# Kernel tuning notes

Hardware: AMD Instinct MI355X
Metric: run time of the kernel (lower is better)

## Reference

```python
import jax, jax.numpy as jnp
import numpy as np

H = 1024      # hidden_size
V = 32000     # vocab_size
MAX_LEN = 32  # decode steps
B = 64        # batch


def _uni(key, shape, s):
    return jax.random.uniform(key, shape, jnp.float32, -s, s)


def setup_inputs() -> dict:
    key = jax.random.key(0)
    ks = jax.random.split(key, 10)
    s = 1.0 / np.sqrt(H)
    return {
        "vectors": jax.random.normal(ks[0], (B, H), jnp.float32),
        "W_fc_in": _uni(ks[1], (H, H), s),
        "b_fc_in": _uni(ks[2], (H,), s),
        "W_ih": _uni(ks[3], (3 * H, H), s),   # torch GRU weight_ih_l0 (r,z,n)
        "W_hh": _uni(ks[4], (3 * H, H), s),
        "b_ih": _uni(ks[5], (3 * H,), s),
        "b_hh": _uni(ks[6], (3 * H,), s),
        "W_out": _uni(ks[7], (V, H), s),
        "b_out": _uni(ks[8], (V,), s),
        "top_k": 8,
    }


def reference(vectors, W_fc_in, b_fc_in, W_ih, W_hh, b_ih, b_hh, W_out, b_out, top_k):
    # hidden = fc_in(vectors); initial GRU input is zeros
    h0 = vectors @ W_fc_in.T + b_fc_in           # [B, H]
    x0 = jnp.zeros_like(h0)

    def gru_cell(carry, _):
        h, x = carry
        gi = x @ W_ih.T + b_ih                   # [B, 3H]
        gh = h @ W_hh.T + b_hh                   # [B, 3H]
        i_r, i_z, i_n = jnp.split(gi, 3, axis=-1)
        h_r, h_z, h_n = jnp.split(gh, 3, axis=-1)
        r = jax.nn.sigmoid(i_r + h_r)
        z = jax.nn.sigmoid(i_z + h_z)
        n = jnp.tanh(i_n + r * h_n)
        h_new = (1.0 - z) * n + z * h            # PyTorch GRU update
        # out == h_new for single-layer GRU; inputs = out feeds back
        return (h_new, h_new), h_new

    _, outs = jax.lax.scan(gru_cell, (h0, x0), None, length=MAX_LEN)  # [T, B, H]

    # fc_out + log_softmax over vocab, for all steps at once
    logits = jnp.einsum('tbh,vh->tbv', outs, W_out) + b_out           # [T, B, V]
    logp = jax.nn.log_softmax(logits, axis=-1)

    # topk then multinomial over exp(top logp) == categorical over top logp
    top_p, top_i = jax.lax.top_k(logp, top_k)                         # [T, B, K]
    samp = jax.random.categorical(jax.random.key(42), top_p, axis=-1)  # [T, B]
    tokens = jnp.take_along_axis(top_i, samp[..., None], axis=-1)[..., 0]
    return tokens.T.astype(jnp.int32)                                  # [B, T]
```

## Files before the change

### kernel.cpp

```cpp
#include <hip/hip_runtime.h>
#include <stdint.h>

typedef unsigned int u32;
typedef unsigned long long u64;
typedef unsigned short ushort;
typedef __attribute__((ext_vector_type(8))) short bf16x8;
typedef __attribute__((ext_vector_type(4))) float f32x4;

#define JAX_PARTITIONABLE 1

#define HD     1024
#define BBATCH 64
#define TSTEP  32
#define VOCAB  32000
#define NROWS  2048
#define GATE6  6144
#define NCB    250
#define NCAND  16

__device__ __forceinline__ void threefry2x32(u32 k0, u32 k1, u32 x0, u32 x1,
                                             u32& y0, u32& y1) {
  u32 ks2 = k0 ^ k1 ^ 0x1BD11BDAu;
  x0 += k0; x1 += k1;
#define TFR(r) do { x0 += x1; x1 = (x1 << (r)) | (x1 >> (32 - (r))); x1 ^= x0; } while (0)
  TFR(13); TFR(15); TFR(26); TFR(6);   x0 += k1;  x1 += ks2 + 1u;
  TFR(17); TFR(29); TFR(16); TFR(24);  x0 += ks2; x1 += k0 + 2u;
  TFR(13); TFR(15); TFR(26); TFR(6);   x0 += k0;  x1 += k1 + 3u;
  TFR(17); TFR(29); TFR(16); TFR(24);  x0 += k1;  x1 += ks2 + 4u;
  TFR(13); TFR(15); TFR(26); TFR(6);   x0 += ks2; x1 += k0 + 5u;
#undef TFR
  y0 = x0; y1 = x1;
}

__device__ __forceinline__ u32 jax_random_bits(u32 n) {
#if JAX_PARTITIONABLE
  u32 y0, y1; threefry2x32(0u, 42u, 0u, n, y0, y1);
  return y0 ^ y1;
#else
  u32 y0, y1;
  if (n < 8192u) { threefry2x32(0u, 42u, n, n + 8192u, y0, y1); return y0; }
  else           { threefry2x32(0u, 42u, n - 8192u, n, y0, y1); return y1; }
#endif
}

__device__ __forceinline__ u64 packkey(float v, int idx) {
  u32 b = __float_as_uint(v);
  b = (b & 0x80000000u) ? ~b : (b | 0x80000000u);
  return ((u64)b << 32) | (u64)(~(u32)idx);
}

__device__ __forceinline__ void insert4(u64* t4, u64 k) {
  if (k > t4[3]) {
    t4[3] = k;
    if (t4[3] > t4[2]) { u64 tm = t4[2]; t4[2] = t4[3]; t4[3] = tm; }
    if (t4[2] > t4[1]) { u64 tm = t4[1]; t4[1] = t4[2]; t4[2] = tm; }
    if (t4[1] > t4[0]) { u64 tm = t4[0]; t4[0] = t4[1]; t4[1] = tm; }
  }
}

__device__ __forceinline__ ushort f2bf_rne(float x) {
  u32 u = __float_as_uint(x);
  return (ushort)((u + 0x7fffu + ((u >> 16) & 1u)) >> 16);
}
__device__ __forceinline__ float bf2f(ushort h) {
  return __uint_as_float(((u32)h) << 16);
}

typedef const __attribute__((address_space(1))) void* gas_ptr;
typedef __attribute__((address_space(3))) void* las_ptr;
__device__ __forceinline__ void gload16(const void* g, void* l) {
  __builtin_amdgcn_global_load_lds((gas_ptr)g, (las_ptr)l, 16, 0, 0);
}

__global__ __launch_bounds__(256) void tobf16(const float* __restrict__ src,
                                              ushort* __restrict__ dst, int n8) {
  int i = blockIdx.x * 256 + threadIdx.x;
  const int stride = gridDim.x * 256;
  for (; i < n8; i += stride) {
    const float4* s4 = (const float4*)src + (size_t)i * 2;
    float4 a = s4[0], b = s4[1];
    u32 o0 = f2bf_rne(a.x) | ((u32)f2bf_rne(a.y) << 16);
    u32 o1 = f2bf_rne(a.z) | ((u32)f2bf_rne(a.w) << 16);
    u32 o2 = f2bf_rne(b.x) | ((u32)f2bf_rne(b.y) << 16);
    u32 o3 = f2bf_rne(b.z) | ((u32)f2bf_rne(b.w) << 16);
    ((uint4*)dst)[i] = make_uint4(o0, o1, o2, o3);
  }
}

__global__ __launch_bounds__(256) void tobf16x3_gru(
    const float* __restrict__ Wih, const float* __restrict__ Whh,
    ushort* __restrict__ w1, ushort* __restrict__ w2, ushort* __restrict__ w3,
    int n8) {
  int i = blockIdx.x * 256 + threadIdx.x;
  const int stride = gridDim.x * 256;
  const int half = 3072 * HD / 8;
  for (; i < n8; i += stride) {
    const float4* s4 = (i < half) ? ((const float4*)Wih + (size_t)i * 2)
                                  : ((const float4*)Whh + (size_t)(i - half) * 2);
    float v[8];
    float4 a = s4[0], b = s4[1];
    v[0]=a.x; v[1]=a.y; v[2]=a.z; v[3]=a.w; v[4]=b.x; v[5]=b.y; v[6]=b.z; v[7]=b.w;
    ushort p1[8], p2[8], p3[8];
#pragma unroll
    for (int e = 0; e < 8; ++e) {
      p1[e] = f2bf_rne(v[e]);
      float r1 = v[e] - bf2f(p1[e]);
      p2[e] = f2bf_rne(r1);
      float r2 = r1 - bf2f(p2[e]);
      p3[e] = f2bf_rne(r2);
    }
    u32 o1[4], o2[4], o3[4];
#pragma unroll
    for (int e = 0; e < 4; ++e) {
      o1[e] = p1[2*e] | ((u32)p1[2*e+1] << 16);
      o2[e] = p2[2*e] | ((u32)p2[2*e+1] << 16);
      o3[e] = p3[2*e] | ((u32)p3[2*e+1] << 16);
    }
    ((uint4*)w1)[i] = make_uint4(o1[0], o1[1], o1[2], o1[3]);
    ((uint4*)w2)[i] = make_uint4(o2[0], o2[1], o2[2], o2[3]);
    ((uint4*)w3)[i] = make_uint4(o3[0], o3[1], o3[2], o3[3]);
  }
}

__global__ __launch_bounds__(256) void gemm64_nt(
    const float* __restrict__ A, const float* __restrict__ B,
    float* __restrict__ part) {
  __shared__ float4 As4[64 * 33];
  __shared__ float4 Bs4[32 * 33];
  const int tid = threadIdx.x;
  const int n0 = blockIdx.x * 32;
  const float* Brow = B + (size_t)n0 * HD;
  const int ks = blockIdx.y * 256;
  const int tc = tid & 7, trg = tid >> 3;
  float acc[2][4] = {};
  for (int kc = 0; kc < 2; ++kc) {
    const int k0 = ks + kc * 128;
#pragma unroll
    for (int l = 0; l < 8; ++l) {
      int m = tid + l * 256; int row = m >> 5, k4 = m & 31;
      As4[row * 33 + k4] = *(const float4*)(A + (size_t)row * HD + k0 + k4 * 4);
    }
#pragma unroll
    for (int l = 0; l < 4; ++l) {
      int m = tid + l * 256; int row = m >> 5, k4 = m & 31;
      Bs4[row * 33 + k4] = *(const float4*)(Brow + (size_t)row * HD + k0 + k4 * 4);
    }
    __syncthreads();
#pragma unroll
    for (int kq = 0; kq < 32; ++kq) {
      float4 av[2], bv[4];
      av[0] = As4[trg * 33 + kq];
      av[1] = As4[(trg + 32) * 33 + kq];
      bv[0] = Bs4[tc * 33 + kq];
      bv[1] = Bs4[(tc + 8) * 33 + kq];
      bv[2] = Bs4[(tc + 16) * 33 + kq];
      bv[3] = Bs4[(tc + 24) * 33 + kq];
#pragma unroll
      for (int i = 0; i < 2; ++i)
#pragma unroll
        for (int j = 0; j < 4; ++j) {
          acc[i][j] += av[i].x * bv[j].x;
          acc[i][j] += av[i].y * bv[j].y;
          acc[i][j] += av[i].z * bv[j].z;
          acc[i][j] += av[i].w * bv[j].w;
        }
    }
    __syncthreads();
  }
  float* P = part + (size_t)blockIdx.y * BBATCH * HD;
#pragma unroll
  for (int i = 0; i < 2; ++i) {
    int b = trg + 32 * i;
#pragma unroll
    for (int j = 0; j < 4; ++j)
      P[(size_t)b * HD + n0 + tc + 8 * j] = acc[i][j];
  }
}

__global__ __launch_bounds__(256) void combine_fcin(
    const float* __restrict__ part, const float* __restrict__ b_fc,
    float* __restrict__ h, ushort* __restrict__ h1, ushort* __restrict__ h2,
    ushort* __restrict__ h3) {
  int idx = blockIdx.x * 256 + threadIdx.x;
  int j = idx & 1023; int b = idx >> 10;
  const size_t S = (size_t)BBATCH * HD;
  const float* p = part + (size_t)b * HD;
  float d = p[j]; d += p[S + j]; d += p[2 * S + j]; d += p[3 * S + j];
  float hv = d + b_fc[j];
  h[idx] = hv;
  ushort a = f2bf_rne(hv);
  float r1 = hv - bf2f(a);
  ushort bb = f2bf_rne(r1);
  float r2 = r1 - bf2f(bb);
  h1[idx] = a; h2[idx] = bb; h3[idx] = f2bf_rne(r2);
}

__global__ __launch_bounds__(256) void gru_gemm(
    const ushort* __restrict__ h1, const ushort* __restrict__ h2,
    const ushort* __restrict__ h3,
    const ushort* __restrict__ W1, const ushort* __restrict__ W2,
    const ushort* __restrict__ W3,
    int colBase, float* __restrict__ g2) {
  __shared__ ushort A1s[64 * 64], A2s[64 * 64], A3s[64 * 64];
  __shared__ ushort B1s[32 * 64], B2s[32 * 64], B3s[32 * 64];
  const int tid = threadIdx.x;
  const int lane = tid & 63, wid = tid >> 6;
  const int wr = wid >> 1, wc = wid & 1;
  const int n0 = colBase + blockIdx.x * 32;
  const int kb0 = blockIdx.y * 512;
  const ushort* B1g = W1 + (size_t)n0 * HD;
  const ushort* B2g = W2 + (size_t)n0 * HD;
  const ushort* B3g = W3 + (size_t)n0 * HD;
  const int rc = lane >> 3;
  const int gr8 = ((lane & 7) ^ rc) * 8;
  const int l15 = lane & 15;
  const int kseg = (lane >> 4) * 16;

  f32x4 acc[2];
  acc[0] = (f32x4){0.f, 0.f, 0.f, 0.f};
  acc[1] = (f32x4){0.f, 0.f, 0.f, 0.f};

  for (int kt = 0; kt < 8; ++kt) {
    const int k0 = kb0 + kt * 64;
#pragma unroll
    for (int c = 0; c < 9; ++c) {
      int q = wid * 9 + c;
      const ushort* src; ushort* dst; int cl;
      if (q < 8)       { cl = q;      src = h1 + (size_t)(cl*8+rc) * HD;  dst = A1s + cl*512; }
      else if (q < 16) { cl = q - 8;  src = h2 + (size_t)(cl*8+rc) * HD;  dst = A2s + cl*512; }
      else if (q < 24) { cl = q - 16; src = h3 + (size_t)(cl*8+rc) * HD;  dst = A3s + cl*512; }
      else if (q < 28) { cl = q - 24; src = B1g + (size_t)(cl*8+rc) * HD; dst = B1s + cl*512; }
      else if (q < 32) { cl = q - 28; src = B2g + (size_t)(cl*8+rc) * HD; dst = B2s + cl*512; }
      else             { cl = q - 32; src = B3g + (size_t)(cl*8+rc) * HD; dst = B3s + cl*512; }
      gload16(src + k0 + gr8, dst);
    }
    asm volatile("s_waitcnt vmcnt(0)" ::: "memory");
    __syncthreads();
#pragma unroll
    for (int ks = 0; ks < 2; ++ks) {
      const int kb = ks * 64 + kseg;
      bf16x8 a1[2], a2[2], a3[2], b1, b2, b3;
#pragma unroll
      for (int m = 0; m < 2; ++m) {
        int row = wr * 32 + m * 16 + l15;
        int off = row * 128 + (kb ^ ((row & 7) << 4));
        a1[m] = *(const bf16x8*)((const char*)A1s + off);
        a2[m] = *(const bf16x8*)((const char*)A2s + off);
        a3[m] = *(const bf16x8*)((const char*)A3s + off);
      }
      {
        int row = wc * 16 + l15;
        int off = row * 128 + (kb ^ ((row & 7) << 4));
        b1 = *(const bf16x8*)((const char*)B1s + off);
        b2 = *(const bf16x8*)((const char*)B2s + off);
        b3 = *(const bf16x8*)((const char*)B3s + off);
      }
#pragma unroll
      for (int m = 0; m < 2; ++m) {
        acc[m] = __builtin_amdgcn_mfma_f32_16x16x32_bf16(a3[m], b1, acc[m], 0, 0, 0);
        acc[m] = __builtin_amdgcn_mfma_f32_16x16x32_bf16(a1[m], b3, acc[m], 0, 0, 0);
        acc[m] = __builtin_amdgcn_mfma_f32_16x16x32_bf16(a2[m], b2, acc[m], 0, 0, 0);
        acc[m] = __builtin_amdgcn_mfma_f32_16x16x32_bf16(a2[m], b1, acc[m], 0, 0, 0);
        acc[m] = __builtin_amdgcn_mfma_f32_16x16x32_bf16(a1[m], b2, acc[m], 0, 0, 0);
        acc[m] = __builtin_amdgcn_mfma_f32_16x16x32_bf16(a1[m], b1, acc[m], 0, 0, 0);
      }
    }
    __syncthreads();
  }
  float* G = g2 + (size_t)blockIdx.y * BBATCH * GATE6;
#pragma unroll
  for (int m = 0; m < 2; ++m)
#pragma unroll
    for (int j = 0; j < 4; ++j) {
      int row = wr * 32 + m * 16 + (lane >> 4) * 4 + j;
      int col = n0 + wc * 16 + l15;
      G[(size_t)row * GATE6 + col] = acc[m][j];
    }
}

__global__ __launch_bounds__(256) void gru_gate2(
    const float* __restrict__ g2, const float* __restrict__ b_ih,
    const float* __restrict__ b_hh, float* __restrict__ h,
    float* __restrict__ outs, ushort* __restrict__ outs_bf,
    ushort* __restrict__ h1, ushort* __restrict__ h2, ushort* __restrict__ h3,
    int t, int first) {
  int idx = blockIdx.x * 256 + threadIdx.x;
  int b = idx >> 10, j = idx & 1023;
  const size_t S = (size_t)BBATCH * GATE6;
  const float* p = g2 + (size_t)b * GATE6;
  float gir, giz, gin;
  if (first) {
    gir = b_ih[j]; giz = b_ih[HD + j]; gin = b_ih[2 * HD + j];
  } else {
    gir = p[j]        + p[S + j]        + b_ih[j];
    giz = p[HD + j]   + p[S + HD + j]   + b_ih[HD + j];
    gin = p[2*HD + j] + p[S + 2*HD + j] + b_ih[2 * HD + j];
  }
  float ghr = p[3072 + j]        + p[S + 3072 + j]        + b_hh[j];
  float ghz = p[3072 + HD + j]   + p[S + 3072 + HD + j]   + b_hh[HD + j];
  float ghn = p[3072 + 2*HD + j] + p[S + 3072 + 2*HD + j] + b_hh[2 * HD + j];
  float r = 1.0f / (1.0f + expf(-(gir + ghr)));
  float z = 1.0f / (1.0f + expf(-(giz + ghz)));
  float n = tanhf(gin + r * ghn);
  float hp = h[idx];
  float hn = (1.0f - z) * n + z * hp;
  h[idx] = hn;
  size_t o = ((size_t)t * BBATCH + b) * HD + j;
  outs[o] = hn;
  ushort a = f2bf_rne(hn);
  outs_bf[o] = a;
  float r1 = hn - bf2f(a);
  ushort bb = f2bf_rne(r1);
  float r2 = r1 - bf2f(bb);
  h1[idx] = a; h2[idx] = bb; h3[idx] = f2bf_rne(r2);
}

__global__ __launch_bounds__(256) void gemm_out_mfma(
    const ushort* __restrict__ Abf, const ushort* __restrict__ Bbf,
    const float* __restrict__ b_out, u64* __restrict__ keys) {
  __shared__ ushort Asm[128 * 64];
  __shared__ ushort Bsm[128 * 64];
  __shared__ float Cs[32 * 133];
  __shared__ u64 pk[64 * 4];

  const int tid = threadIdx.x;
  const int lane = tid & 63;
  const int wid = tid >> 6;
  const int wr = wid >> 1, wc = wid & 1;
  const int cb = blockIdx.y;
  const int half = blockIdx.x;
  const int n0 = cb * 128;

  const ushort* Bg = Bbf + (size_t)n0 * HD;
  const int rc = lane >> 3;
  const int gr8 = ((lane & 7) ^ rc) * 8;
  const int l15 = lane & 15;
  const int kseg = (lane >> 4) * 16;

  float bo[4];
#pragma unroll
  for (int n = 0; n < 4; ++n) bo[n] = b_out[n0 + wc * 64 + n * 16 + l15];

  for (int rb = 0; rb < 8; ++rb) {
    const int r0 = (half * 8 + rb) * 128;
    const ushort* Ag = Abf + (size_t)r0 * HD;

    f32x4 acc[4][4];
#pragma unroll
    for (int m = 0; m < 4; ++m)
#pragma unroll
      for (int n = 0; n < 4; ++n) acc[m][n] = (f32x4){0.f, 0.f, 0.f, 0.f};

    for (int kt = 0; kt < 16; ++kt) {
      const int k0 = kt * 64;
#pragma unroll
      for (int c = 0; c < 4; ++c) {
        int ch = wid * 4 + c;
        int row = ch * 8 + rc;
        gload16(Ag + (size_t)row * HD + k0 + gr8, Asm + ch * 512);
        gload16(Bg + (size_t)row * HD + k0 + gr8, Bsm + ch * 512);
      }
      asm volatile("s_waitcnt vmcnt(0)" ::: "memory");
      __syncthreads();
#pragma unroll
      for (int ks = 0; ks < 2; ++ks) {
        bf16x8 a[4], b[4];
#pragma unroll
        for (int m = 0; m < 4; ++m) {
          int row = wr * 64 + m * 16 + l15;
          int kb = ks * 64 + kseg;
          int off = row * 128 + (kb ^ ((row & 7) << 4));
          a[m] = *(const bf16x8*)((const char*)Asm + off);
        }
#pragma unroll
        for (int n = 0; n < 4; ++n) {
          int row = wc * 64 + n * 16 + l15;
          int kb = ks * 64 + kseg;
          int off = row * 128 + (kb ^ ((row & 7) << 4));
          b[n] = *(const bf16x8*)((const char*)Bsm + off);
        }
#pragma unroll
        for (int m = 0; m < 4; ++m)
#pragma unroll
          for (int n = 0; n < 4; ++n)
            acc[m][n] = __builtin_amdgcn_mfma_f32_16x16x32_bf16(a[m], b[n], acc[m][n], 0, 0, 0);
      }
      __syncthreads();
    }

    for (int q = 0; q < 4; ++q) {
      if (wr == (q >> 1)) {
        int mbase = (q & 1) * 2;
#pragma unroll
        for (int mi = 0; mi < 2; ++mi) {
          int m = mbase + mi;
#pragma unroll
          for (int n = 0; n < 4; ++n) {
            int c = wc * 64 + n * 16 + l15;
#pragma unroll
            for (int j = 0; j < 4; ++j) {
              int lr = mi * 16 + (lane >> 4) * 4 + j;
              Cs[lr * 133 + c] = acc[m][n][j] + bo[n];
            }
          }
        }
      }
      __syncthreads();
      if (tid < 64) {
        int rr = tid >> 1, hc = (tid & 1) * 64;
        const float* rp = Cs + rr * 133 + hc;
        u64 t4[4] = {0, 0, 0, 0};
        for (int c = 0; c < 64; ++c) insert4(t4, packkey(rp[c], n0 + hc + c));
        u64* d = pk + tid * 4;
        d[0] = t4[0]; d[1] = t4[1]; d[2] = t4[2]; d[3] = t4[3];
      }
      __syncthreads();
      if (tid < 32) {
        const u64* a4 = pk + tid * 8;
        u64 t4[4] = {a4[0], a4[1], a4[2], a4[3]};
        insert4(t4, a4[4]); insert4(t4, a4[5]); insert4(t4, a4[6]); insert4(t4, a4[7]);
        int grow = r0 + q * 32 + tid;
        u64* kp = keys + ((size_t)grow * NCB + cb) * 4;
        kp[0] = t4[0]; kp[1] = t4[1]; kp[2] = t4[2]; kp[3] = t4[3];
      }
      __syncthreads();
    }
  }
}

__global__ __launch_bounds__(256) void merge_sample2(
    const u64* __restrict__ keys, const float* __restrict__ outs,
    const float* __restrict__ W_out, const float* __restrict__ b_out,
    int* __restrict__ out) {
  const int r = blockIdx.x, tid = threadIdx.x;
  const int lane = tid & 63, wid = tid >> 6;
  __shared__ u64 K[1000];
  __shared__ u64 wmax[4];
  __shared__ u64 topw[NCAND];
  __shared__ float candv[NCAND];
  __shared__ float row_f[1024];
  for (int i = tid; i < 1000; i += 256) K[i] = keys[(size_t)r * 1000 + i];
  for (int i = tid; i < 1024; i += 256) row_f[i] = outs[(size_t)r * 1024 + i];
  __syncthreads();
  for (int it = 0; it < NCAND; ++it) {
    u64 b = 0;
#pragma unroll
    for (int l = 0; l < 4; ++l) {
      int i = tid + l * 256;
      if (i < 1000) { u64 v = K[i]; b = (v > b) ? v : b; }
    }
#pragma unroll
    for (int o = 32; o; o >>= 1) {
      u64 x = __shfl_xor(b, o);
      if (x > b) b = x;
    }
    if (lane == 0) wmax[wid] = b;
    __syncthreads();
    u64 w = wmax[0];
    if (wmax[1] > w) w = wmax[1];
    if (wmax[2] > w) w = wmax[2];
    if (wmax[3] > w) w = wmax[3];
    if (tid == 0) topw[it] = w;
#pragma unroll
    for (int l = 0; l < 4; ++l) {
      int i = tid + l * 256;
      if (i < 1000 && K[i] == w) K[i] = 0;
    }
    __syncthreads();
  }
  {
    int c = tid >> 4, l16 = tid & 15;
    int vidx = (int)(~(u32)(topw[c] & 0xffffffffu));
    const float* wrow = W_out + (size_t)vidx * HD;
    float s = 0.f;
    for (int e = l16; e < 1024; e += 16) s += row_f[e] * wrow[e];
#pragma unroll
    for (int o = 8; o; o >>= 1) s += __shfl_xor(s, o, 16);
    if (l16 == 0) candv[c] = s + b_out[vidx];
  }
  __syncthreads();
  if (tid == 0) {
    float v[NCAND]; int vi[NCAND];
#pragma unroll
    for (int q = 0; q < NCAND; ++q) {
      v[q] = candv[q];
      vi[q] = (int)(~(u32)(topw[q] & 0xffffffffu));
    }
    for (int a = 0; a < 8; ++a)
      for (int b2 = a + 1; b2 < NCAND; ++b2) {
        bool sw = (v[b2] > v[a]) || (v[b2] == v[a] && vi[b2] < vi[a]);
        if (sw) {
          float tf = v[a]; v[a] = v[b2]; v[b2] = tf;
          int ti = vi[a]; vi[a] = vi[b2]; vi[b2] = ti;
        }
      }
    const float M = v[0];
    const float TINY = 1.17549435e-38f;
    float best = -3.4e38f; int bi = 0;
    for (int k = 0; k < 8; ++k) {
      float lp = v[k] - M;
      u32 bits = jax_random_bits((u32)(r * 8 + k));
      float f = __uint_as_float((bits >> 9) | 0x3f800000u) - 1.0f;
      float u = f * (1.0f - TINY) + TINY;
      u = fmaxf(TINY, u);
      float g = -logf(-logf(u));
      float s = g + lp;
      if (s > best) { best = s; bi = k; }
    }
    int t = r >> 6, b = r & 63;
    out[b * TSTEP + t] = vi[bi];
  }
}

extern "C" void kernel_launch(void* const* d_in, const int* in_sizes, int n_in,
                              void* d_out, int out_size, void* d_ws, size_t ws_size,
                              hipStream_t stream) {
  (void)in_sizes; (void)n_in; (void)out_size; (void)ws_size;
  const float* vectors = (const float*)d_in[0];
  const float* W_fc_in = (const float*)d_in[1];
  const float* b_fc_in = (const float*)d_in[2];
  const float* W_ih    = (const float*)d_in[3];
  const float* W_hh    = (const float*)d_in[4];
  const float* b_ih    = (const float*)d_in[5];
  const float* b_hh    = (const float*)d_in[6];
  const float* W_out   = (const float*)d_in[7];
  const float* b_out   = (const float*)d_in[8];
  int* out = (int*)d_out;

  char* w = (char*)d_ws;
  float* h = (float*)w;          w += (size_t)BBATCH * HD * 4;
  float* outs = (float*)w;       w += (size_t)NROWS * HD * 4;
  ushort* outs_bf = (ushort*)w;  w += (size_t)NROWS * HD * 2;
  ushort* Wbf = (ushort*)w;      w += (size_t)VOCAB * HD * 2;
  char* X = w;                   w += (size_t)3 * GATE6 * HD * 2;
  ushort* Wg1 = (ushort*)X;
  ushort* Wg2 = Wg1 + (size_t)GATE6 * HD;
  ushort* Wg3 = Wg2 + (size_t)GATE6 * HD;
  u64* keys = (u64*)X;
  ushort* h1 = (ushort*)w;       w += (size_t)BBATCH * HD * 2;
  ushort* h2 = (ushort*)w;       w += (size_t)BBATCH * HD * 2;
  ushort* h3 = (ushort*)w;       w += (size_t)BBATCH * HD * 2;
  float* part = (float*)w;
  float* g2   = (float*)w;

  tobf16<<<4096, 256, 0, stream>>>(W_out, Wbf, VOCAB * HD / 8);
  tobf16x3_gru<<<1024, 256, 0, stream>>>(W_ih, W_hh, Wg1, Wg2, Wg3, GATE6 * HD / 8);

  gemm64_nt<<<dim3(32, 4), 256, 0, stream>>>(vectors, W_fc_in, part);
  combine_fcin<<<256, 256, 0, stream>>>(part, b_fc_in, h, h1, h2, h3);

  for (int t = 0; t < TSTEP; ++t) {
    if (t == 0)
      gru_gemm<<<dim3(96, 2), 256, 0, stream>>>(h1, h2, h3, Wg1, Wg2, Wg3, 3072, g2);
    else
      gru_gemm<<<dim3(192, 2), 256, 0, stream>>>(h1, h2, h3, Wg1, Wg2, Wg3, 0, g2);
    gru_gate2<<<256, 256, 0, stream>>>(g2, b_ih, b_hh, h, outs, outs_bf,
                                       h1, h2, h3, t, t == 0 ? 1 : 0);
  }

  gemm_out_mfma<<<dim3(2, NCB), 256, 0, stream>>>(outs_bf, Wbf, b_out, keys);

  merge_sample2<<<NROWS, 256, 0, stream>>>(keys, outs, W_out, b_out, out);
}
```

Measured before the change: 1.257 ms.

## Fuse GRU steps into persistent kernel with grid barriers; double-buffer output GEMM

Replaces the 64 per-step GEMM and gate launches with one persistent kernel of 384 blocks. Each block computes its gate GEMM tile, waits at a hierarchical atomic grid barrier, applies the gate update, then waits at a second barrier. This removes kernel launch overhead and gaps between steps, but relies on all 384 blocks being resident at once, since the barrier could deadlock otherwise. Separately, the vocab-projection GEMM now uses 32-wide k-tiles double-buffered in LDS with a new swizzle, so global loads overlap MFMA compute.

Result: slower. 4.815 ms (+283.2%).

```diff
diff --git a/kernel.cpp b/kernel.cpp
--- a/kernel.cpp
+++ b/kernel.cpp
@@ -17,6 +17,7 @@
 #define GATE6  6144
 #define NCB    250
 #define NCAND  16
+#define GRU_BLOCKS 384
 
 __device__ __forceinline__ void threefry2x32(u32 k0, u32 k1, u32 x0, u32 x1,
                                              u32& y0, u32& y1) {
@@ -70,6 +71,36 @@
 typedef __attribute__((address_space(3))) void* las_ptr;
 __device__ __forceinline__ void gload16(const void* g, void* l) {
   __builtin_amdgcn_global_load_lds((gas_ptr)g, (las_ptr)l, 16, 0, 0);
+}
+
+__device__ __forceinline__ void grid_bar2(u32* B, int nPerGrp) {
+  __syncthreads();
+  if (threadIdx.x == 0) {
+    __threadfence();
+    const int g = blockIdx.x & 7;
+    u32* gc = B + g * 32;
+    u32* gg = B + 256 + g * 32;
+    u32 mygen = __hip_atomic_load(gg, __ATOMIC_RELAXED, __HIP_MEMORY_SCOPE_AGENT);
+    u32 a = __hip_atomic_fetch_add(gc, 1u, __ATOMIC_ACQ_REL, __HIP_MEMORY_SCOPE_AGENT);
+    if (a == (u32)nPerGrp - 1) {
+      __hip_atomic_store(gc, 0u, __ATOMIC_RELAXED, __HIP_MEMORY_SCOPE_AGENT);
+      u32* GC = B + 512; u32* GG = B + 544;
+      u32 mg = __hip_atomic_load(GG, __ATOMIC_RELAXED, __HIP_MEMORY_SCOPE_AGENT);
+      u32 ga = __hip_atomic_fetch_add(GC, 1u, __ATOMIC_ACQ_REL, __HIP_MEMORY_SCOPE_AGENT);
+      if (ga == 7u) {
+        __hip_atomic_store(GC, 0u, __ATOMIC_RELAXED, __HIP_MEMORY_SCOPE_AGENT);
+        __hip_atomic_fetch_add(GG, 1u, __ATOMIC_RELEASE, __HIP_MEMORY_SCOPE_AGENT);
+      } else {
+        while (__hip_atomic_load(GG, __ATOMIC_ACQUIRE, __HIP_MEMORY_SCOPE_AGENT) == mg)
+          __builtin_amdgcn_s_sleep(1);
+      }
+      __hip_atomic_fetch_add(gg, 1u, __ATOMIC_RELEASE, __HIP_MEMORY_SCOPE_AGENT);
+    } else {
+      while (__hip_atomic_load(gg, __ATOMIC_ACQUIRE, __HIP_MEMORY_SCOPE_AGENT) == mygen)
+        __builtin_amdgcn_s_sleep(1);
+    }
+  }
+  __syncthreads();
 }
 
 __global__ __launch_bounds__(256) void tobf16(const float* __restrict__ src,
@@ -195,19 +226,23 @@
   h1[idx] = a; h2[idx] = bb; h3[idx] = f2bf_rne(r2);
 }
 
-__global__ __launch_bounds__(256) void gru_gemm(
-    const ushort* __restrict__ h1, const ushort* __restrict__ h2,
-    const ushort* __restrict__ h3,
+__global__ __launch_bounds__(256, 2) void gru_fused(
     const ushort* __restrict__ W1, const ushort* __restrict__ W2,
     const ushort* __restrict__ W3,
-    int colBase, float* __restrict__ g2) {
+    const float* __restrict__ b_ih, const float* __restrict__ b_hh,
+    float* __restrict__ h, float* __restrict__ outs,
+    ushort* __restrict__ outs_bf,
+    ushort* __restrict__ h1, ushort* __restrict__ h2, ushort* __restrict__ h3,
+    float* __restrict__ g2, u32* __restrict__ bar) {
   __shared__ ushort A1s[64 * 64], A2s[64 * 64], A3s[64 * 64];
   __shared__ ushort B1s[32 * 64], B2s[32 * 64], B3s[32 * 64];
   const int tid = threadIdx.x;
   const int lane = tid & 63, wid = tid >> 6;
   const int wr = wid >> 1, wc = wid & 1;
-  const int n0 = colBase + blockIdx.x * 32;
-  const int kb0 = blockIdx.y * 512;
+  const int bid = blockIdx.x;
+  const int n0 = (bid >> 1) * 32;
+  const int ksplit = bid & 1;
+  const int kb0 = ksplit * 512;
   const ushort* B1g = W1 + (size_t)n0 * HD;
   const ushort* B2g = W2 + (size_t)n0 * HD;
   const ushort* B3g = W3 + (size_t)n0 * HD;
@@ -215,111 +250,111 @@
   const int gr8 = ((lane & 7) ^ rc) * 8;
   const int l15 = lane & 15;
   const int kseg = (lane >> 4) * 16;
-
-  f32x4 acc[2];
-  acc[0] = (f32x4){0.f, 0.f, 0.f, 0.f};
-  acc[1] = (f32x4){0.f, 0.f, 0.f, 0.f};
-
-  for (int kt = 0; kt < 8; ++kt) {
-    const int k0 = kb0 + kt * 64;
-#pragma unroll
-    for (int c = 0; c < 9; ++c) {
-      int q = wid * 9 + c;
-      const ushort* src; ushort* dst; int cl;
-      if (q < 8)       { cl = q;      src = h1 + (size_t)(cl*8+rc) * HD;  dst = A1s + cl*512; }
-      else if (q < 16) { cl = q - 8;  src = h2 + (size_t)(cl*8+rc) * HD;  dst = A2s + cl*512; }
-      else if (q < 24) { cl = q - 16; src = h3 + (size_t)(cl*8+rc) * HD;  dst = A3s + cl*512; }
-      else if (q < 28) { cl = q - 24; src = B1g + (size_t)(cl*8+rc) * HD; dst = B1s + cl*512; }
-      else if (q < 32) { cl = q - 28; src = B2g + (size_t)(cl*8+rc) * HD; dst = B2s + cl*512; }
-      else             { cl = q - 32; src = B3g + (size_t)(cl*8+rc) * HD; dst = B3s + cl*512; }
-      gload16(src + k0 + gr8, dst);
-    }
-    asm volatile("s_waitcnt vmcnt(0)" ::: "memory");
-    __syncthreads();
-#pragma unroll
-    for (int ks = 0; ks < 2; ++ks) {
-      const int kb = ks * 64 + kseg;
-      bf16x8 a1[2], a2[2], a3[2], b1, b2, b3;
-#pragma unroll
-      for (int m = 0; m < 2; ++m) {
-        int row = wr * 32 + m * 16 + l15;
-        int off = row * 128 + (kb ^ ((row & 7) << 4));
-        a1[m] = *(const bf16x8*)((const char*)A1s + off);
-        a2[m] = *(const bf16x8*)((const char*)A2s + off);
-        a3[m] = *(const bf16x8*)((const char*)A3s + off);
+  const int gidx = bid * 256 + tid;
+  const size_t S = (size_t)BBATCH * GATE6;
+
+  for (int t = 0; t < TSTEP; ++t) {
+    if (t > 0 || n0 >= 3072) {
+      f32x4 acc[2];
+      acc[0] = (f32x4){0.f, 0.f, 0.f, 0.f};
+      acc[1] = (f32x4){0.f, 0.f, 0.f, 0.f};
+      for (int kt = 0; kt < 8; ++kt) {
+        const int k0 = kb0 + kt * 64;
+#pragma unroll
+        for (int c = 0; c < 9; ++c) {
+          int q = wid * 9 + c;
+          const ushort* src; ushort* dst; int cl;
+          if (q < 8)       { cl = q;      src = h1 + (size_t)(cl*8+rc) * HD;  dst = A1s + cl*512; }
+          else if (q < 16) { cl = q - 8;  src = h2 + (size_t)(cl*8+rc) * HD;  dst = A2s + cl*512; }
+          else if (q < 24) { cl = q - 16; src = h3 + (size_t)(cl*8+rc) * HD;  dst = A3s + cl*512; }
+          else if (q < 28) { cl = q - 24; src = B1g + (size_t)(cl*8+rc) * HD; dst = B1s + cl*512; }
+          else if (q < 32) { cl = q - 28; src = B2g + (size_t)(cl*8+rc) * HD; dst = B2s + cl*512; }
+          else             { cl = q - 32; src = B3g + (size_t)(cl*8+rc) * HD; dst = B3s + cl*512; }
+          gload16(src + k0 + gr8, dst);
+        }
+        asm volatile("s_waitcnt vmcnt(0)" ::: "memory");
+        __syncthreads();
+#pragma unroll
+        for (int ks = 0; ks < 2; ++ks) {
+          const int kb = ks * 64 + kseg;
+          bf16x8 a1[2], a2[2], a3[2], b1, b2, b3;
+#pragma unroll
+          for (int m = 0; m < 2; ++m) {
+            int row = wr * 32 + m * 16 + l15;
+            int off = row * 128 + (kb ^ ((row & 7) << 4));
+            a1[m] = *(const bf16x8*)((const char*)A1s + off);
+            a2[m] = *(const bf16x8*)((const char*)A2s + off);
+            a3[m] = *(const bf16x8*)((const char*)A3s + off);
+          }
+          {
+            int row = wc * 16 + l15;
+            int off = row * 128 + (kb ^ ((row & 7) << 4));
+            b1 = *(const bf16x8*)((const char*)B1s + off);
+            b2 = *(const bf16x8*)((const char*)B2s + off);
+            b3 = *(const bf16x8*)((const char*)B3s + off);
+          }
+#pragma unroll
+          for (int m = 0; m < 2; ++m) {
+            acc[m] = __builtin_amdgcn_mfma_f32_16x16x32_bf16(a3[m], b1, acc[m], 0, 0, 0);
+            acc[m] = __builtin_amdgcn_mfma_f32_16x16x32_bf16(a1[m], b3, acc[m], 0, 0, 0);
+            acc[m] = __builtin_amdgcn_mfma_f32_16x16x32_bf16(a2[m], b2, acc[m], 0, 0, 0);
+            acc[m] = __builtin_amdgcn_mfma_f32_16x16x32_bf16(a2[m], b1, acc[m], 0, 0, 0);
+            acc[m] = __builtin_amdgcn_mfma_f32_16x16x32_bf16(a1[m], b2, acc[m], 0, 0, 0);
+            acc[m] = __builtin_amdgcn_mfma_f32_16x16x32_bf16(a1[m], b1, acc[m], 0, 0, 0);
+          }
+        }
+        __syncthreads();
       }
-      {
-        int row = wc * 16 + l15;
-        int off = row * 128 + (kb ^ ((row & 7) << 4));
-        b1 = *(const bf16x8*)((const char*)B1s + off);
-        b2 = *(const bf16x8*)((const char*)B2s + off);
-        b3 = *(const bf16x8*)((const char*)B3s + off);
+      float* G = g2 + (size_t)ksplit * BBATCH * GATE6;
+#pragma unroll
+      for (int m = 0; m < 2; ++m)
+#pragma unroll
+        for (int j = 0; j < 4; ++j) {
+          int row = wr * 32 + m * 16 + (lane >> 4) * 4 + j;
+          int col = n0 + wc * 16 + l15;
+          G[(size_t)row * GATE6 + col] = acc[m][j];
+        }
+    }
+    grid_bar2(bar, GRU_BLOCKS / 8);
+
+    if (gidx < BBATCH * HD) {
+      int b = gidx >> 10, j = gidx & 1023;
+      const float* p = g2 + (size_t)b * GATE6;
+      float gir, giz, gin;
+      if (t == 0) {
+        gir = b_ih[j]; giz = b_ih[HD + j]; gin = b_ih[2 * HD + j];
+      } else {
+        gir = p[j]        + p[S + j]        + b_ih[j];
+        giz = p[HD + j]   + p[S + HD + j]   + b_ih[HD + j];
+        gin = p[2*HD + j] + p[S + 2*HD + j] + b_ih[2 * HD + j];
       }
-#pragma unroll
-      for (int m = 0; m < 2; ++m) {
-        acc[m] = __builtin_amdgcn_mfma_f32_16x16x32_bf16(a3[m], b1, acc[m], 0, 0, 0);
-        acc[m] = __builtin_amdgcn_mfma_f32_16x16x32_bf16(a1[m], b3, acc[m], 0, 0, 0);
-        acc[m] = __builtin_amdgcn_mfma_f32_16x16x32_bf16(a2[m], b2, acc[m], 0, 0, 0);
-        acc[m] = __builtin_amdgcn_mfma_f32_16x16x32_bf16(a2[m], b1, acc[m], 0, 0, 0);
-        acc[m] = __builtin_amdgcn_mfma_f32_16x16x32_bf16(a1[m], b2, acc[m], 0, 0, 0);
-        acc[m] = __builtin_amdgcn_mfma_f32_16x16x32_bf16(a1[m], b1, acc[m], 0, 0, 0);
-      }
-    }
-    __syncthreads();
-  }
-  float* G = g2 + (size_t)blockIdx.y * BBATCH * GATE6;
-#pragma unroll
-  for (int m = 0; m < 2; ++m)
-#pragma unroll
-    for (int j = 0; j < 4; ++j) {
-      int row = wr * 32 + m * 16 + (lane >> 4) * 4 + j;
-      int col = n0 + wc * 16 + l15;
-      G[(size_t)row * GATE6 + col] = acc[m][j];
-    }
-}
-
-__global__ __launch_bounds__(256) void gru_gate2(
-    const float* __restrict__ g2, const float* __restrict__ b_ih,
-    const float* __restrict__ b_hh, float* __restrict__ h,
-    float* __restrict__ outs, ushort* __restrict__ outs_bf,
-    ushort* __restrict__ h1, ushort* __restrict__ h2, ushort* __restrict__ h3,
-    int t, int first) {
-  int idx = blockIdx.x * 256 + threadIdx.x;
-  int b = idx >> 10, j = idx & 1023;
-  const size_t S = (size_t)BBATCH * GATE6;
-  const float* p = g2 + (size_t)b * GATE6;
-  float gir, giz, gin;
-  if (first) {
-    gir = b_ih[j]; giz = b_ih[HD + j]; gin = b_ih[2 * HD + j];
-  } else {
-    gir = p[j]        + p[S + j]        + b_ih[j];
-    giz = p[HD + j]   + p[S + HD + j]   + b_ih[HD + j];
-    gin = p[2*HD + j] + p[S + 2*HD + j] + b_ih[2 * HD + j];
-  }
-  float ghr = p[3072 + j]        + p[S + 3072 + j]        + b_hh[j];
-  float ghz = p[3072 + HD + j]   + p[S + 3072 + HD + j]   + b_hh[HD + j];
-  float ghn = p[3072 + 2*HD + j] + p[S + 3072 + 2*HD + j] + b_hh[2 * HD + j];
-  float r = 1.0f / (1.0f + expf(-(gir + ghr)));
-  float z = 1.0f / (1.0f + expf(-(giz + ghz)));
-  float n = tanhf(gin + r * ghn);
-  float hp = h[idx];
-  float hn = (1.0f - z) * n + z * hp;
-  h[idx] = hn;
-  size_t o = ((size_t)t * BBATCH + b) * HD + j;
-  outs[o] = hn;
-  ushort a = f2bf_rne(hn);
-  outs_bf[o] = a;
-  float r1 = hn - bf2f(a);
-  ushort bb = f2bf_rne(r1);
-  float r2 = r1 - bf2f(bb);
-  h1[idx] = a; h2[idx] = bb; h3[idx] = f2bf_rne(r2);
+      float ghr = p[3072 + j]        + p[S + 3072 + j]        + b_hh[j];
+      float ghz = p[3072 + HD + j]   + p[S + 3072 + HD + j]   + b_hh[HD + j];
+      float ghn = p[3072 + 2*HD + j] + p[S + 3072 + 2*HD + j] + b_hh[2 * HD + j];
+      float r = 1.0f / (1.0f + expf(-(gir + ghr)));
+      float z = 1.0f / (1.0f + expf(-(giz + ghz)));
+      float n = tanhf(gin + r * ghn);
+      float hp = h[gidx];
+      float hn = (1.0f - z) * n + z * hp;
+      h[gidx] = hn;
+      size_t o = ((size_t)t * BBATCH + b) * HD + j;
+      outs[o] = hn;
+      ushort a = f2bf_rne(hn);
+      outs_bf[o] = a;
+      float r1 = hn - bf2f(a);
+      ushort bb = f2bf_rne(r1);
+      float r2 = r1 - bf2f(bb);
+      h1[gidx] = a; h2[gidx] = bb; h3[gidx] = f2bf_rne(r2);
+    }
+    grid_bar2(bar, GRU_BLOCKS / 8);
+  }
 }
 
 __global__ __launch_bounds__(256) void gemm_out_mfma(
     const ushort* __restrict__ Abf, const ushort* __restrict__ Bbf,
     const float* __restrict__ b_out, u64* __restrict__ keys) {
-  __shared__ ushort Asm[128 * 64];
-  __shared__ ushort Bsm[128 * 64];
+  __shared__ ushort Ab0[128 * 32], Ab1[128 * 32];
+  __shared__ ushort Bb0[128 * 32], Bb1[128 * 32];
   __shared__ float Cs[32 * 133];
   __shared__ u64 pk[64 * 4];
 
@@ -332,10 +367,38 @@
   const int n0 = cb * 128;
 
   const ushort* Bg = Bbf + (size_t)n0 * HD;
-  const int rc = lane >> 3;
-  const int gr8 = ((lane & 7) ^ rc) * 8;
+  const int rc4 = lane >> 2;
+  const int gs8 = ((lane & 3) ^ ((lane >> 3) & 3)) * 8;
   const int l15 = lane & 15;
-  const int kseg = (lane >> 4) * 16;
+  const int swoff = (((lane >> 4) ^ ((l15 >> 1) & 3)) << 4);
+
+#define STAGE_OUT(AB, BB, k0) do {                                   \
+    _Pragma("unroll")                                                \
+    for (int c_ = 0; c_ < 2; ++c_) {                                 \
+      int ch_ = wid * 2 + c_;                                        \
+      int row_ = ch_ * 16 + rc4;                                     \
+      gload16(Ag + (size_t)row_ * HD + (k0) + gs8, (AB) + ch_ * 512);\
+      gload16(Bg + (size_t)row_ * HD + (k0) + gs8, (BB) + ch_ * 512);\
+    }                                                                \
+  } while (0)
+
+#define COMPUTE_OUT(AB, BB) do {                                     \
+    bf16x8 a_[4], b_[4];                                             \
+    _Pragma("unroll")                                                \
+    for (int m_ = 0; m_ < 4; ++m_)                                   \
+      a_[m_] = *(const bf16x8*)((const char*)(AB) +                  \
+               (wr * 64 + m_ * 16 + l15) * 64 + swoff);              \
+    _Pragma("unroll")                                                \
+    for (int n_ = 0; n_ < 4; ++n_)                                   \
+      b_[n_] = *(const bf16x8*)((const char*)(BB) +                  \
+               (wc * 64 + n_ * 16 + l15) * 64 + swoff);              \
+    _Pragma("unroll")                                                \
+    for (int m_ = 0; m_ < 4; ++m_)                                   \
+      _Pragma("unroll")                                              \
+      for (int n_ = 0; n_ < 4; ++n_)                                 \
+        acc[m_][n_] = __builtin_amdgcn_mfma_f32_16x16x32_bf16(       \
+            a_[m_], b_[n_], acc[m_][n_], 0, 0, 0);                   \
+  } while (0)
 
   float bo[4];
 #pragma unroll
@@ -351,40 +414,17 @@
 #pragma unroll
       for (int n = 0; n < 4; ++n) acc[m][n] = (f32x4){0.f, 0.f, 0.f, 0.f};
 
-    for (int kt = 0; kt < 16; ++kt) {
-      const int k0 = kt * 64;
-#pragma unroll
-      for (int c = 0; c < 4; ++c) {
-        int ch = wid * 4 + c;
-        int row = ch * 8 + rc;
-        gload16(Ag + (size_t)row * HD + k0 + gr8, Asm + ch * 512);
-        gload16(Bg + (size_t)row * HD + k0 + gr8, Bsm + ch * 512);
-      }
+    STAGE_OUT(Ab0, Bb0, 0);
+    asm volatile("s_waitcnt vmcnt(0)" ::: "memory");
+    __syncthreads();
+    for (int kp = 0; kp < 16; ++kp) {
+      STAGE_OUT(Ab1, Bb1, (2 * kp + 1) * 32);
+      COMPUTE_OUT(Ab0, Bb0);
       asm volatile("s_waitcnt vmcnt(0)" ::: "memory");
       __syncthreads();
-#pragma unroll
-      for (int ks = 0; ks < 2; ++ks) {
-        bf16x8 a[4], b[4];
-#pragma unroll
-        for (int m = 0; m < 4; ++m) {
-          int row = wr * 64 + m * 16 + l15;
-          int kb = ks * 64 + kseg;
-          int off = row * 128 + (kb ^ ((row & 7) << 4));
-          a[m] = *(const bf16x8*)((const char*)Asm + off);
-        }
-#pragma unroll
-        for (int n = 0; n < 4; ++n) {
-          int row = wc * 64 + n * 16 + l15;
-          int kb = ks * 64 + kseg;
-          int off = row * 128 + (kb ^ ((row & 7) << 4));
-          b[n] = *(const bf16x8*)((const char*)Bsm + off);
-        }
-#pragma unroll
-        for (int m = 0; m < 4; ++m)
-#pragma unroll
-          for (int n = 0; n < 4; ++n)
-            acc[m][n] = __builtin_amdgcn_mfma_f32_16x16x32_bf16(a[m], b[n], acc[m][n], 0, 0, 0);
-      }
+      if (kp < 15) STAGE_OUT(Ab0, Bb0, (2 * kp + 2) * 32);
+      COMPUTE_OUT(Ab1, Bb1);
+      asm volatile("s_waitcnt vmcnt(0)" ::: "memory");
       __syncthreads();
     }
 
@@ -420,12 +460,14 @@
         u64 t4[4] = {a4[0], a4[1], a4[2], a4[3]};
         insert4(t4, a4[4]); insert4(t4, a4[5]); insert4(t4, a4[6]); insert4(t4, a4[7]);
         int grow = r0 + q * 32 + tid;
-        u64* kp = keys + ((size_t)grow * NCB + cb) * 4;
-        kp[0] = t4[0]; kp[1] = t4[1]; kp[2] = t4[2]; kp[3] = t4[3];
+        u64* kp2 = keys + ((size_t)grow * NCB + cb) * 4;
+        kp2[0] = t4[0]; kp2[1] = t4[1]; kp2[2] = t4[2]; kp2[3] = t4[3];
       }
       __syncthreads();
     }
   }
+#undef STAGE_OUT
+#undef COMPUTE_OUT
 }
 
 __global__ __launch_bounds__(256) void merge_sample2(
@@ -540,23 +582,21 @@
   ushort* h1 = (ushort*)w;       w += (size_t)BBATCH * HD * 2;
   ushort* h2 = (ushort*)w;       w += (size_t)BBATCH * HD * 2;
   ushort* h3 = (ushort*)w;       w += (size_t)BBATCH * HD * 2;
+  u32* bar = (u32*)w;            w += 4096;
   float* part = (float*)w;
   float* g2   = (float*)w;
 
+  hipMemsetAsync(bar, 0, 4096, stream);
+
   tobf16<<<4096, 256, 0, stream>>>(W_out, Wbf, VOCAB * HD / 8);
   tobf16x3_gru<<<1024, 256, 0, stream>>>(W_ih, W_hh, Wg1, Wg2, Wg3, GATE6 * HD / 8);
 
   gemm64_nt<<<dim3(32, 4), 256, 0, stream>>>(vectors, W_fc_in, part);
   combine_fcin<<<256, 256, 0, stream>>>(part, b_fc_in, h, h1, h2, h3);
 
-  for (int t = 0; t < TSTEP; ++t) {
-    if (t == 0)
-      gru_gemm<<<dim3(96, 2), 256, 0, stream>>>(h1, h2, h3, Wg1, Wg2, Wg3, 3072, g2);
-    else
-      gru_gemm<<<dim3(192, 2), 256, 0, stream>>>(h1, h2, h3, Wg1, Wg2, Wg3, 0, g2);
-    gru_gate2<<<256, 256, 0, stream>>>(g2, b_ih, b_hh, h, outs, outs_bf,
-                                       h1, h2, h3, t, t == 0 ? 1 : 0);
-  }
+  gru_fused<<<GRU_BLOCKS, 256, 0, stream>>>(Wg1, Wg2, Wg3, b_ih, b_hh,
+                                            h, outs, outs_bf, h1, h2, h3,
+                                            g2, bar);
 
   gemm_out_mfma<<<dim3(2, NCB), 256, 0, stream>>>(outs_bf, Wbf, b_out, keys);
 
```
